# Optimization experiments

Hardware: AMD Instinct MI355X
Metric: run time of the kernel (lower is better)

The kernel has to match this reference:

```python
import jax, jax.numpy as jnp
import numpy as np

BN_EPS = 1e-5


def _gru(x, Wih, Whh, bih, bhh):
    # x: [B,S,D]; Wih: [3H,D]; Whh: [3H,H]; PyTorch gate order (r, z, n)
    B, S, D = x.shape
    H = Whh.shape[1]
    xg = jnp.einsum('bsd,gd->bsg', x, Wih) + bih  # [B,S,3H] precomputed input gates

    def step(h, xg_t):
        hg = h @ Whh.T + bhh
        xr, xz, xn = jnp.split(xg_t, 3, axis=-1)
        hr, hz, hn = jnp.split(hg, 3, axis=-1)
        r = jax.nn.sigmoid(xr + hr)
        z = jax.nn.sigmoid(xz + hz)
        n = jnp.tanh(xn + r * hn)
        h_new = (1.0 - z) * n + z * h
        return h_new, h_new

    h0 = jnp.zeros((B, H), x.dtype)
    _, hs = jax.lax.scan(step, h0, jnp.swapaxes(xg, 0, 1))  # [S,B,H]
    return jnp.swapaxes(hs, 0, 1)


def _lstm(x, Wih, Whh, bih, bhh):
    # x: [B,S,D]; PyTorch gate order (i, f, g, o)
    B, S, D = x.shape
    H = Whh.shape[1]
    xg = jnp.einsum('bsd,gd->bsg', x, Wih) + bih  # [B,S,4H]

    def step(carry, xg_t):
        h, c = carry
        g = xg_t + h @ Whh.T + bhh
        i, f, gg, o = jnp.split(g, 4, axis=-1)
        i = jax.nn.sigmoid(i)
        f = jax.nn.sigmoid(f)
        gg = jnp.tanh(gg)
        o = jax.nn.sigmoid(o)
        c_new = f * c + i * gg
        h_new = o * jnp.tanh(c_new)
        return (h_new, c_new), h_new

    h0 = jnp.zeros((B, H), x.dtype)
    c0 = jnp.zeros((B, H), x.dtype)
    _, hs = jax.lax.scan(step, (h0, c0), jnp.swapaxes(xg, 0, 1))
    return jnp.swapaxes(hs, 0, 1)


def setup_inputs() -> dict:
    key = jax.random.key(0)
    B, S, D, H = 64, 512, 40, 512
    ks = jax.random.split(key, 16)
    s_in = 1.0 / np.sqrt(H)

    def u(k, shape):
        return jax.random.uniform(k, shape, jnp.float32, -s_in, s_in)

    inp = {
        'x': jax.random.normal(ks[0], (B, S, D), jnp.float32),
        # rec1: GRU
        'gru_Wih': u(ks[1], (3 * H, D)),
        'gru_Whh': u(ks[2], (3 * H, H)),
        'gru_bih': u(ks[3], (3 * H,)),
        'gru_bhh': u(ks[4], (3 * H,)),
        # rec2: LSTM over [x, ssr] -> input D+1
        'lstm_Wih': u(ks[5], (4 * H, D + 1)),
        'lstm_Whh': u(ks[6], (4 * H, H)),
        'lstm_bih': u(ks[7], (4 * H,)),
        'lstm_bhh': u(ks[8], (4 * H,)),
        # fc1/fc2/fc3: hidden -> 1
        'fc1_w': u(ks[9], (1, H)), 'fc1_b': u(ks[10], (1,)),
        'fc2_w': u(ks[11], (1, H)), 'fc2_b': u(ks[12], (1,)),
        'fc3_w': u(ks[13], (1, H)), 'fc3_b': u(ks[14], (1,)),
        # BatchNorm1d affine params
        'bn_gamma': jnp.ones((H,), jnp.float32),
        'bn_beta': jnp.zeros((H,), jnp.float32),
    }
    return inp


def reference(x, gru_Wih, gru_Whh, gru_bih, gru_bhh,
              lstm_Wih, lstm_Whh, lstm_bih, lstm_bhh,
              fc1_w, fc1_b, fc2_w, fc2_b, fc3_w, fc3_b,
              bn_gamma, bn_beta):
    B, S, D = x.shape
    o1 = _gru(x, gru_Wih, gru_Whh, gru_bih, gru_bhh)  # [B,S,H]
    # BatchNorm1d (training mode): per-channel stats over (batch, time)
    mean = jnp.mean(o1, axis=(0, 1))
    var = jnp.mean((o1 - mean) ** 2, axis=(0, 1))
    o1 = (o1 - mean) * jax.lax.rsqrt(var + BN_EPS) * bn_gamma + bn_beta
    # gated scalar channel (dropout p=0 is identity)
    sr = jax.nn.relu(o1 @ fc1_w.T + fc1_b)            # [B,S,1]
    w = jnp.abs(jax.nn.sigmoid(o1 @ fc2_w.T + fc2_b))  # [B,S,1]
    ssr = sr * (w + 1.0)                              # [B,S,1]
    x2 = jnp.concatenate([x, ssr], axis=2)            # [B,S,D+1]
    o2 = _lstm(x2, lstm_Wih, lstm_Whh, lstm_bih, lstm_bhh)
    out = jax.nn.relu(o2 @ fc3_w.T + fc3_b)           # [B,S,1]
    return out, ssr
```

## Files before the change

kernel.cpp:

```cpp
#include <hip/hip_runtime.h>
#include <stdint.h>

#define MB 16
#define GW 16
#define NU 32
#define HD 512
#define SEQ 512
#define DX 40

using short8 = __attribute__((ext_vector_type(8))) short;
using f32x4  = __attribute__((ext_vector_type(4))) float;

__device__ __forceinline__ unsigned short f2bf(float f) {
  uint32_t u = __builtin_bit_cast(uint32_t, f);
  u += 0x7fffu + ((u >> 16) & 1u);
  return (unsigned short)(u >> 16);
}
__device__ __forceinline__ float sigm(float x) { return 1.0f / (1.0f + __expf(-x)); }


__global__ __launch_bounds__(512, 2) void gru_kernel(
    const float* __restrict__ x, const float* __restrict__ Wih,
    const float* __restrict__ Whh, const float* __restrict__ bih,
    const float* __restrict__ bhh, unsigned* __restrict__ flags,
    unsigned short* __restrict__ hbuf, float* __restrict__ o1,
    float* __restrict__ stats)
{
  const int wg = blockIdx.x & (GW - 1);
  const int g  = blockIdx.x >> 4;
  const int tid = threadIdx.x;
  const int wave = tid >> 6;
  const int lane = tid & 63;
  const int u0 = wg * NU;
  const int bg = g * MB;

  __shared__ unsigned short h_s[MB][520];
  __shared__ unsigned short x_s[MB][72];
  __shared__ float gate_s[3][MB][NU];
  __shared__ float xn_s[MB][NU];

  for (int i = tid; i < MB * 32; i += 512) x_s[i >> 5][40 + (i & 31)] = 0;

  short8 bfrag[18];
  const int myGate = wave >> 1;
  const int ut = wave & 1;
  const int kq = (lane >> 4) * 8;
  if (wave < 6) {
    const int row = myGate * HD + u0 + ut * 16 + (lane & 15);
    for (int kt = 0; kt < 16; ++kt) {
      const float* p = Whh + (size_t)row * HD + kt * 32 + kq;
      short8 f;
#pragma unroll
      for (int j = 0; j < 8; ++j) f[j] = (short)f2bf(p[j]);
      bfrag[kt] = f;
    }
    for (int kt = 16; kt < 18; ++kt) {
      short8 f;
#pragma unroll
      for (int j = 0; j < 8; ++j) {
        int c = kt * 32 + kq + j - HD;
        float v = (myGate < 2 && c < DX) ? Wih[(size_t)row * DX + c] : 0.0f;
        f[j] = (short)f2bf(v);
      }
      bfrag[kt] = f;
    }
  } else {
    const int row = 2 * HD + u0 + (wave - 6) * 16 + (lane & 15);
    for (int kt = 0; kt < 2; ++kt) {
      short8 f;
#pragma unroll
      for (int j = 0; j < 8; ++j) {
        int c = kt * 32 + kq + j;
        f[j] = (short)((c < DX) ? f2bf(Wih[(size_t)row * DX + c]) : 0);
      }
      bfrag[kt] = f;
    }
  }

  const int sb = tid >> 5;
  const int su = tid & 31;
  float hprev = 0.0f, ssum = 0.0f, ssq = 0.0f;
  const float b_r  = bih[u0 + su] + bhh[u0 + su];
  const float b_z  = bih[HD + u0 + su] + bhh[HD + u0 + su];
  const float b_in = bih[2 * HD + u0 + su];
  const float b_hn = bhh[2 * HD + u0 + su];

  unsigned* gf = flags + g * GW * 16;
  unsigned* myProdFlag = gf + ((tid & 127) >> 3) * 16;

  for (int t = 0; t < SEQ; ++t) {
    const unsigned long long* hin64 =
        (const unsigned long long*)(hbuf + ((size_t)g * 2 + (t & 1)) * MB * HD);
    uint32_t* hout32 =
        (uint32_t*)(hbuf + ((size_t)g * 2 + ((t + 1) & 1)) * MB * HD);

    {
      while (__hip_atomic_load(myProdFlag, __ATOMIC_RELAXED,
                               __HIP_MEMORY_SCOPE_AGENT) < (unsigned)t)
        __builtin_amdgcn_s_sleep(1);
#pragma unroll
      for (int it = 0; it < 4; ++it) {
        int q = it * 512 + tid;
        unsigned long long v = __hip_atomic_load(hin64 + q, __ATOMIC_RELAXED,
                                                 __HIP_MEMORY_SCOPE_AGENT);
        *(unsigned long long*)(&h_s[q >> 7][(q & 127) * 4]) = v;
      }
    }
    {
      int b = tid >> 5, c = tid & 31;
      const float* xr = x + ((size_t)(bg + b) * SEQ + t) * DX;
      x_s[b][c] = f2bf(xr[c]);
      if (c < 8) x_s[b][32 + c] = f2bf(xr[32 + c]);
    }
    __syncthreads();

    if (wave < 6) {
      const int m = lane & 15;
      f32x4 acc = {0.f, 0.f, 0.f, 0.f};
#pragma unroll
      for (int kt = 0; kt < 16; ++kt) {
        short8 a = *(const short8*)(&h_s[m][kt * 32 + kq]);
        acc = __builtin_amdgcn_mfma_f32_16x16x32_bf16(a, bfrag[kt], acc, 0, 0, 0);
      }
      short8 ax0 = *(const short8*)(&x_s[m][kq]);
      short8 ax1 = *(const short8*)(&x_s[m][32 + kq]);
      acc = __builtin_amdgcn_mfma_f32_16x16x32_bf16(ax0, bfrag[16], acc, 0, 0, 0);
      acc = __builtin_amdgcn_mfma_f32_16x16x32_bf16(ax1, bfrag[17], acc, 0, 0, 0);
#pragma unroll
      for (int r = 0; r < 4; ++r)
        gate_s[myGate][(lane >> 4) * 4 + r][ut * 16 + (lane & 15)] = acc[r];
    } else {
      const int m = lane & 15;
      f32x4 acc = {0.f, 0.f, 0.f, 0.f};
      short8 ax0 = *(const short8*)(&x_s[m][kq]);
      short8 ax1 = *(const short8*)(&x_s[m][32 + kq]);
      acc = __builtin_amdgcn_mfma_f32_16x16x32_bf16(ax0, bfrag[0], acc, 0, 0, 0);
      acc = __builtin_amdgcn_mfma_f32_16x16x32_bf16(ax1, bfrag[1], acc, 0, 0, 0);
#pragma unroll
      for (int r = 0; r < 4; ++r)
        xn_s[(lane >> 4) * 4 + r][(wave - 6) * 16 + (lane & 15)] = acc[r];
    }
    __syncthreads();

    float r_ = sigm(gate_s[0][sb][su] + b_r);
    float z_ = sigm(gate_s[1][sb][su] + b_z);
    float n_ = tanhf(xn_s[sb][su] + b_in + r_ * (gate_s[2][sb][su] + b_hn));
    float h = (1.0f - z_) * n_ + z_ * hprev;
    hprev = h;
    ssum += h; ssq += h * h;
    {
      float hp = __shfl_xor(h, 1);
      if ((tid & 1) == 0) {
        uint32_t packed = (uint32_t)f2bf(h) | ((uint32_t)f2bf(hp) << 16);
        __hip_atomic_store(hout32 + ((sb * HD + u0 + su) >> 1), packed,
                           __ATOMIC_RELAXED, __HIP_MEMORY_SCOPE_AGENT);
      }
    }
    __syncthreads();

    if (tid == 0)
      __hip_atomic_store(gf + wg * 16, (unsigned)(t + 1), __ATOMIC_RELAXED,
                         __HIP_MEMORY_SCOPE_AGENT);
    o1[((size_t)(bg + sb) * SEQ + t) * HD + u0 + su] = h;
  }

  atomicAdd(&stats[u0 + su], ssum);
  atomicAdd(&stats[HD + u0 + su], ssq);
}

__global__ __launch_bounds__(512, 2) void lstm_kernel(
    const float* __restrict__ x, const float* __restrict__ Wih,
    const float* __restrict__ Whh, const float* __restrict__ bih,
    const float* __restrict__ bhh, const float* __restrict__ ssr,
    unsigned* __restrict__ flags, unsigned short* __restrict__ hbuf,
    float* __restrict__ o2)
{
  const int wg = blockIdx.x & (GW - 1);
  const int g  = blockIdx.x >> 4;
  const int tid = threadIdx.x;
  const int wave = tid >> 6;
  const int lane = tid & 63;
  const int u0 = wg * NU;
  const int bg = g * MB;

  __shared__ unsigned short h_s[MB][520];
  __shared__ unsigned short x_s[MB][72];
  __shared__ float gate_s[4][MB][NU];

  for (int i = tid; i < MB * 32; i += 512) x_s[i >> 5][40 + (i & 31)] = 0;

  short8 bfrag[18];
  const int myGate = wave >> 1;
  const int ut = wave & 1;
  const int kq = (lane >> 4) * 8;
  {
    const int row = myGate * HD + u0 + ut * 16 + (lane & 15);
    for (int kt = 0; kt < 16; ++kt) {
      const float* p = Whh + (size_t)row * HD + kt * 32 + kq;
      short8 f;
#pragma unroll
      for (int j = 0; j < 8; ++j) f[j] = (short)f2bf(p[j]);
      bfrag[kt] = f;
    }
    for (int kt = 16; kt < 18; ++kt) {
      short8 f;
#pragma unroll
      for (int j = 0; j < 8; ++j) {
        int c = kt * 32 + kq + j - HD;
        float v = (c < 41) ? Wih[(size_t)row * 41 + c] : 0.0f;
        f[j] = (short)f2bf(v);
      }
      bfrag[kt] = f;
    }
  }

  const int sb = tid >> 5;
  const int su = tid & 31;
  float creg = 0.0f;
  const float b_i = bih[u0 + su] + bhh[u0 + su];
  const float b_f = bih[HD + u0 + su] + bhh[HD + u0 + su];
  const float b_g = bih[2 * HD + u0 + su] + bhh[2 * HD + u0 + su];
  const float b_o = bih[3 * HD + u0 + su] + bhh[3 * HD + u0 + su];

  unsigned* gf = flags + g * GW * 16;
  unsigned* myProdFlag = gf + ((tid & 127) >> 3) * 16;

  for (int t = 0; t < SEQ; ++t) {
    const unsigned long long* hin64 =
        (const unsigned long long*)(hbuf + ((size_t)g * 2 + (t & 1)) * MB * HD);
    uint32_t* hout32 =
        (uint32_t*)(hbuf + ((size_t)g * 2 + ((t + 1) & 1)) * MB * HD);

    {
      while (__hip_atomic_load(myProdFlag, __ATOMIC_RELAXED,
                               __HIP_MEMORY_SCOPE_AGENT) < (unsigned)t)
        __builtin_amdgcn_s_sleep(1);
#pragma unroll
      for (int it = 0; it < 4; ++it) {
        int q = it * 512 + tid;
        unsigned long long v = __hip_atomic_load(hin64 + q, __ATOMIC_RELAXED,
                                                 __HIP_MEMORY_SCOPE_AGENT);
        *(unsigned long long*)(&h_s[q >> 7][(q & 127) * 4]) = v;
      }
    }
    {
      int b = tid >> 5, c = tid & 31;
      const float* xr = x + ((size_t)(bg + b) * SEQ + t) * DX;
      x_s[b][c] = f2bf(xr[c]);
      if (c < 8) x_s[b][32 + c] = f2bf(xr[32 + c]);
      if (c == 8) x_s[b][40] = f2bf(ssr[(size_t)(bg + b) * SEQ + t]);
    }
    __syncthreads();

    {
      const int m = lane & 15;
      f32x4 acc = {0.f, 0.f, 0.f, 0.f};
#pragma unroll
      for (int kt = 0; kt < 16; ++kt) {
        short8 a = *(const short8*)(&h_s[m][kt * 32 + kq]);
        acc = __builtin_amdgcn_mfma_f32_16x16x32_bf16(a, bfrag[kt], acc, 0, 0, 0);
      }
      short8 ax0 = *(const short8*)(&x_s[m][kq]);
      short8 ax1 = *(const short8*)(&x_s[m][32 + kq]);
      acc = __builtin_amdgcn_mfma_f32_16x16x32_bf16(ax0, bfrag[16], acc, 0, 0, 0);
      acc = __builtin_amdgcn_mfma_f32_16x16x32_bf16(ax1, bfrag[17], acc, 0, 0, 0);
#pragma unroll
      for (int r = 0; r < 4; ++r)
        gate_s[myGate][(lane >> 4) * 4 + r][ut * 16 + (lane & 15)] = acc[r];
    }
    __syncthreads();

    float gi = sigm(gate_s[0][sb][su] + b_i);
    float gf_ = sigm(gate_s[1][sb][su] + b_f);
    float gg = tanhf(gate_s[2][sb][su] + b_g);
    float go = sigm(gate_s[3][sb][su] + b_o);
    creg = gf_ * creg + gi * gg;
    float h = go * tanhf(creg);
    {
      float hp = __shfl_xor(h, 1);
      if ((tid & 1) == 0) {
        uint32_t packed = (uint32_t)f2bf(h) | ((uint32_t)f2bf(hp) << 16);
        __hip_atomic_store(hout32 + ((sb * HD + u0 + su) >> 1), packed,
                           __ATOMIC_RELAXED, __HIP_MEMORY_SCOPE_AGENT);
      }
    }
    __syncthreads();

    if (tid == 0)
      __hip_atomic_store(gf + wg * 16, (unsigned)(t + 1), __ATOMIC_RELAXED,
                         __HIP_MEMORY_SCOPE_AGENT);
    o2[((size_t)(bg + sb) * SEQ + t) * HD + u0 + su] = h;
  }
}

__global__ __launch_bounds__(512) void coef_kernel(
    const float* __restrict__ stats, const float* __restrict__ fc1_w,
    const float* __restrict__ fc1_b, const float* __restrict__ fc2_w,
    const float* __restrict__ fc2_b, const float* __restrict__ gamma,
    const float* __restrict__ beta, float* __restrict__ coef)
{
  __shared__ float r1[512], r2[512];
  const int j = threadIdx.x;
  const float inv_n = 1.0f / 32768.0f;
  float mean = stats[j] * inv_n;
  float var = stats[HD + j] * inv_n - mean * mean;
  float scale = gamma[j] * rsqrtf(var + 1e-5f);
  float shift = beta[j] - mean * scale;
  coef[j] = fc1_w[j] * scale;
  coef[HD + j] = fc2_w[j] * scale;
  r1[j] = fc1_w[j] * shift;
  r2[j] = fc2_w[j] * shift;
  __syncthreads();
  for (int s = 256; s > 0; s >>= 1) {
    if (j < s) { r1[j] += r1[j + s]; r2[j] += r2[j + s]; }
    __syncthreads();
  }
  if (j == 0) {
    coef[2 * HD] = r1[0] + fc1_b[0];
    coef[2 * HD + 1] = r2[0] + fc2_b[0];
  }
}

__global__ __launch_bounds__(256) void ssr_kernel(
    const float* __restrict__ o1, const float* __restrict__ coef,
    float* __restrict__ ssr_ws, float* __restrict__ dssr)
{
  const int row = blockIdx.x * 4 + (threadIdx.x >> 6);
  const int lane = threadIdx.x & 63;
  const float* p = o1 + (size_t)row * HD + lane * 8;
  float s1 = 0.f, s2 = 0.f;
#pragma unroll
  for (int j = 0; j < 8; ++j) {
    float v = p[j];
    s1 += v * coef[lane * 8 + j];
    s2 += v * coef[HD + lane * 8 + j];
  }
#pragma unroll
  for (int off = 32; off > 0; off >>= 1) {
    s1 += __shfl_down(s1, off);
    s2 += __shfl_down(s2, off);
  }
  if (lane == 0) {
    float sr = fmaxf(s1 + coef[2 * HD], 0.0f);
    float w = fabsf(sigm(s2 + coef[2 * HD + 1]));
    float v = sr * (1.0f + w);
    ssr_ws[row] = v;
    dssr[row] = v;
  }
}

__global__ __launch_bounds__(256) void out_kernel(
    const float* __restrict__ o2, const float* __restrict__ fc3_w,
    const float* __restrict__ fc3_b, float* __restrict__ dout)
{
  const int row = blockIdx.x * 4 + (threadIdx.x >> 6);
  const int lane = threadIdx.x & 63;
  const float* p = o2 + (size_t)row * HD + lane * 8;
  float s = 0.f;
#pragma unroll
  for (int j = 0; j < 8; ++j) s += p[j] * fc3_w[lane * 8 + j];
#pragma unroll
  for (int off = 32; off > 0; off >>= 1) s += __shfl_down(s, off);
  if (lane == 0) dout[row] = fmaxf(s + fc3_b[0], 0.0f);
}

extern "C" void kernel_launch(void* const* d_in, const int* in_sizes, int n_in,
                              void* d_out, int out_size, void* d_ws, size_t ws_size,
                              hipStream_t stream) {
  (void)in_sizes; (void)n_in; (void)out_size; (void)ws_size;
  const float* x    = (const float*)d_in[0];
  const float* gWih = (const float*)d_in[1];
  const float* gWhh = (const float*)d_in[2];
  const float* gbih = (const float*)d_in[3];
  const float* gbhh = (const float*)d_in[4];
  const float* lWih = (const float*)d_in[5];
  const float* lWhh = (const float*)d_in[6];
  const float* lbih = (const float*)d_in[7];
  const float* lbhh = (const float*)d_in[8];
  const float* fc1w = (const float*)d_in[9];
  const float* fc1b = (const float*)d_in[10];
  const float* fc2w = (const float*)d_in[11];
  const float* fc2b = (const float*)d_in[12];
  const float* fc3w = (const float*)d_in[13];
  const float* fc3b = (const float*)d_in[14];
  const float* gam  = (const float*)d_in[15];
  const float* bet  = (const float*)d_in[16];
  float* out = (float*)d_out;

  char* ws = (char*)d_ws;
  unsigned* flags_g = (unsigned*)(ws + 0);
  unsigned* flags_l = (unsigned*)(ws + 4096);
  float* stats      = (float*)(ws + 8192);
  float* coef       = (float*)(ws + 16384);
  float* ssr_ws     = (float*)(ws + 32768);
  unsigned short* hbuf_g = (unsigned short*)(ws + 262144);
  unsigned short* hbuf_l = (unsigned short*)(ws + 393216);
  float* o1 = (float*)(ws + 1048576);
  float* o2 = o1 + (size_t)64 * SEQ * HD;

  hipMemsetAsync(ws, 0, 12288, stream);
  hipMemsetAsync(ws + 262144, 0, 262144, stream);

  gru_kernel<<<dim3(64), dim3(512), 0, stream>>>(x, gWih, gWhh, gbih, gbhh,
                                                 flags_g, hbuf_g, o1, stats);
  coef_kernel<<<dim3(1), dim3(512), 0, stream>>>(stats, fc1w, fc1b, fc2w, fc2b,
                                                 gam, bet, coef);
  ssr_kernel<<<dim3(8192), dim3(256), 0, stream>>>(o1, coef, ssr_ws, out + 32768);
  lstm_kernel<<<dim3(64), dim3(512), 0, stream>>>(x, lWih, lWhh, lbih, lbhh, ssr_ws,
                                                  flags_l, hbuf_l, o2);
  out_kernel<<<dim3(8192), dim3(256), 0, stream>>>(o2, fc3w, fc3b, out);
}
```

Before: 3.304 ms.

## Fuse gate computation per wave and use per-wave flags with double-buffered LDS

Restructures the GRU and LSTM recurrent kernels so each wave computes all gates for its 16 hidden units in registers. This removes the gate_s shared-memory round trip and one of the per-step block barriers. Each wave publishes its own completion flag after a vmcnt wait, instead of one flag per block after a barrier. h and x shared buffers are double-buffered so only one __syncthreads remains per step. The grid shrinks to 32 blocks of 256 threads, with more weight registers per thread, which lowers parallelism and adds more flags to poll.

```diff
diff --git a/kernel.cpp b/kernel.cpp
--- a/kernel.cpp
+++ b/kernel.cpp
@@ -2,14 +2,16 @@
 #include <stdint.h>
 
 #define MB 16
-#define GW 16
-#define NU 32
+#define GW 8
+#define NU 64
 #define HD 512
 #define SEQ 512
 #define DX 40
+#define NPROD 32
 
 using short8 = __attribute__((ext_vector_type(8))) short;
 using f32x4  = __attribute__((ext_vector_type(4))) float;
+typedef unsigned long long ull;
 
 __device__ __forceinline__ unsigned short f2bf(float f) {
   uint32_t u = __builtin_bit_cast(uint32_t, f);
@@ -17,9 +19,14 @@
   return (unsigned short)(u >> 16);
 }
 __device__ __forceinline__ float sigm(float x) { return 1.0f / (1.0f + __expf(-x)); }
-
-
-__global__ __launch_bounds__(512, 2) void gru_kernel(
+__device__ __forceinline__ ull pack4bf(float4 v) {
+  return (ull)f2bf(v.x) | ((ull)f2bf(v.y) << 16) | ((ull)f2bf(v.z) << 32) |
+         ((ull)f2bf(v.w) << 48);
+}
+#define MFMA(a, b, c) __builtin_amdgcn_mfma_f32_16x16x32_bf16((a), (b), (c), 0, 0, 0)
+
+
+__global__ __launch_bounds__(256, 1) void gru_kernel(
     const float* __restrict__ x, const float* __restrict__ Wih,
     const float* __restrict__ Whh, const float* __restrict__ bih,
     const float* __restrict__ bhh, unsigned* __restrict__ flags,
@@ -27,148 +34,138 @@
     float* __restrict__ stats)
 {
   const int wg = blockIdx.x & (GW - 1);
-  const int g  = blockIdx.x >> 4;
+  const int g  = blockIdx.x >> 3;
   const int tid = threadIdx.x;
   const int wave = tid >> 6;
   const int lane = tid & 63;
-  const int u0 = wg * NU;
+  const int n = lane & 15;
+  const int q = lane >> 4;
+  const int kq = q * 8;
+  const int u = wg * NU + wave * 16 + n;
   const int bg = g * MB;
 
-  __shared__ unsigned short h_s[MB][520];
-  __shared__ unsigned short x_s[MB][72];
-  __shared__ float gate_s[3][MB][NU];
-  __shared__ float xn_s[MB][NU];
-
-  for (int i = tid; i < MB * 32; i += 512) x_s[i >> 5][40 + (i & 31)] = 0;
-
-  short8 bfrag[18];
-  const int myGate = wave >> 1;
-  const int ut = wave & 1;
-  const int kq = (lane >> 4) * 8;
-  if (wave < 6) {
-    const int row = myGate * HD + u0 + ut * 16 + (lane & 15);
+  __shared__ unsigned short h_s[2][MB][520];
+  __shared__ unsigned short x_s[2][MB][72];
+
+  for (int i = tid; i < 2 * MB * 24; i += 256) {
+    int pbuf = i / (MB * 24), r = (i / 24) % MB, c = 40 + (i % 24);
+    x_s[pbuf][r][c] = 0;
+  }
+
+  short8 WR[16], WZ[16], WN[16], XR[2], XZ[2], XN[2];
+  for (int kt = 0; kt < 16; ++kt) {
+    const float* pr = Whh + (size_t)(0 * HD + u) * HD + kt * 32 + kq;
+    const float* pz = Whh + (size_t)(1 * HD + u) * HD + kt * 32 + kq;
+    const float* pn = Whh + (size_t)(2 * HD + u) * HD + kt * 32 + kq;
+    short8 fr, fz, fn;
+#pragma unroll
+    for (int j = 0; j < 8; ++j) {
+      fr[j] = (short)f2bf(pr[j]); fz[j] = (short)f2bf(pz[j]);
+      fn[j] = (short)f2bf(pn[j]);
+    }
+    WR[kt] = fr; WZ[kt] = fz; WN[kt] = fn;
+  }
+  for (int kt = 0; kt < 2; ++kt) {
+    short8 fr, fz, fn;
+#pragma unroll
+    for (int j = 0; j < 8; ++j) {
+      int c = kt * 32 + kq + j;
+      float vr = (c < DX) ? Wih[(size_t)(0 * HD + u) * DX + c] : 0.0f;
+      float vz = (c < DX) ? Wih[(size_t)(1 * HD + u) * DX + c] : 0.0f;
+      float vn = (c < DX) ? Wih[(size_t)(2 * HD + u) * DX + c] : 0.0f;
+      fr[j] = (short)f2bf(vr); fz[j] = (short)f2bf(vz); fn[j] = (short)f2bf(vn);
+    }
+    XR[kt] = fr; XZ[kt] = fz; XN[kt] = fn;
+  }
+
+  const float b_r  = bih[u] + bhh[u];
+  const float b_z  = bih[HD + u] + bhh[HD + u];
+  const float b_in = bih[2 * HD + u];
+  const float b_hn = bhh[2 * HD + u];
+
+  float hprev[4] = {0.f, 0.f, 0.f, 0.f};
+  float ssum = 0.f, ssq = 0.f;
+
+  unsigned* gflags   = flags + g * NPROD * 16;
+  unsigned* myflag   = gflags + (wg * 4 + wave) * 16;
+  unsigned* pollflag = gflags + (tid >> 3) * 16;
+  const int sp = tid >> 3;
+  const int sj = tid & 7;
+
+  for (int t = 0; t < SEQ; ++t) {
+    const int pb = t & 1;
+    const ull* hin = (const ull*)(hbuf + ((size_t)g * 2 + pb) * MB * HD);
+    unsigned short* hout = hbuf + ((size_t)g * 2 + (pb ^ 1)) * MB * HD;
+
+    while (__hip_atomic_load(pollflag, __ATOMIC_RELAXED,
+                             __HIP_MEMORY_SCOPE_AGENT) < (unsigned)t)
+      __builtin_amdgcn_s_sleep(1);
+    ull w[8];
+#pragma unroll
+    for (int r2 = 0; r2 < 2; ++r2)
+#pragma unroll
+      for (int c4 = 0; c4 < 4; ++c4)
+        w[r2 * 4 + c4] = __hip_atomic_load(
+            hin + (2 * sj + r2) * 128 + sp * 4 + c4, __ATOMIC_RELAXED,
+            __HIP_MEMORY_SCOPE_AGENT);
+#pragma unroll
+    for (int r2 = 0; r2 < 2; ++r2)
+#pragma unroll
+      for (int c4 = 0; c4 < 4; ++c4)
+        *(ull*)(&h_s[pb][2 * sj + r2][sp * 16 + c4 * 4]) = w[r2 * 4 + c4];
+    {
+      int b = tid >> 4, c = tid & 15;
+      if (c < 10) {
+        float4 v = *(const float4*)(x + ((size_t)(bg + b) * SEQ + t) * DX + c * 4);
+        *(ull*)(&x_s[pb][b][c * 4]) = pack4bf(v);
+      }
+    }
+    __syncthreads();
+
+    f32x4 aR = {0,0,0,0}, aZ = {0,0,0,0}, aN = {0,0,0,0}, aX = {0,0,0,0};
+#pragma unroll
     for (int kt = 0; kt < 16; ++kt) {
-      const float* p = Whh + (size_t)row * HD + kt * 32 + kq;
-      short8 f;
-#pragma unroll
-      for (int j = 0; j < 8; ++j) f[j] = (short)f2bf(p[j]);
-      bfrag[kt] = f;
-    }
-    for (int kt = 16; kt < 18; ++kt) {
-      short8 f;
-#pragma unroll
-      for (int j = 0; j < 8; ++j) {
-        int c = kt * 32 + kq + j - HD;
-        float v = (myGate < 2 && c < DX) ? Wih[(size_t)row * DX + c] : 0.0f;
-        f[j] = (short)f2bf(v);
-      }
-      bfrag[kt] = f;
-    }
-  } else {
-    const int row = 2 * HD + u0 + (wave - 6) * 16 + (lane & 15);
-    for (int kt = 0; kt < 2; ++kt) {
-      short8 f;
-#pragma unroll
-      for (int j = 0; j < 8; ++j) {
-        int c = kt * 32 + kq + j;
-        f[j] = (short)((c < DX) ? f2bf(Wih[(size_t)row * DX + c]) : 0);
-      }
-      bfrag[kt] = f;
-    }
-  }
-
-  const int sb = tid >> 5;
-  const int su = tid & 31;
-  float hprev = 0.0f, ssum = 0.0f, ssq = 0.0f;
-  const float b_r  = bih[u0 + su] + bhh[u0 + su];
-  const float b_z  = bih[HD + u0 + su] + bhh[HD + u0 + su];
-  const float b_in = bih[2 * HD + u0 + su];
-  const float b_hn = bhh[2 * HD + u0 + su];
-
-  unsigned* gf = flags + g * GW * 16;
-  unsigned* myProdFlag = gf + ((tid & 127) >> 3) * 16;
-
-  for (int t = 0; t < SEQ; ++t) {
-    const unsigned long long* hin64 =
-        (const unsigned long long*)(hbuf + ((size_t)g * 2 + (t & 1)) * MB * HD);
-    uint32_t* hout32 =
-        (uint32_t*)(hbuf + ((size_t)g * 2 + ((t + 1) & 1)) * MB * HD);
-
+      short8 a = *(const short8*)(&h_s[pb][n][kt * 32 + kq]);
+      aR = MFMA(a, WR[kt], aR);
+      aZ = MFMA(a, WZ[kt], aZ);
+      aN = MFMA(a, WN[kt], aN);
+    }
     {
-      while (__hip_atomic_load(myProdFlag, __ATOMIC_RELAXED,
-                               __HIP_MEMORY_SCOPE_AGENT) < (unsigned)t)
-        __builtin_amdgcn_s_sleep(1);
-#pragma unroll
-      for (int it = 0; it < 4; ++it) {
-        int q = it * 512 + tid;
-        unsigned long long v = __hip_atomic_load(hin64 + q, __ATOMIC_RELAXED,
-                                                 __HIP_MEMORY_SCOPE_AGENT);
-        *(unsigned long long*)(&h_s[q >> 7][(q & 127) * 4]) = v;
-      }
-    }
-    {
-      int b = tid >> 5, c = tid & 31;
-      const float* xr = x + ((size_t)(bg + b) * SEQ + t) * DX;
-      x_s[b][c] = f2bf(xr[c]);
-      if (c < 8) x_s[b][32 + c] = f2bf(xr[32 + c]);
-    }
-    __syncthreads();
-
-    if (wave < 6) {
-      const int m = lane & 15;
-      f32x4 acc = {0.f, 0.f, 0.f, 0.f};
-#pragma unroll
-      for (int kt = 0; kt < 16; ++kt) {
-        short8 a = *(const short8*)(&h_s[m][kt * 32 + kq]);
-        acc = __builtin_amdgcn_mfma_f32_16x16x32_bf16(a, bfrag[kt], acc, 0, 0, 0);
-      }
-      short8 ax0 = *(const short8*)(&x_s[m][kq]);
-      short8 ax1 = *(const short8*)(&x_s[m][32 + kq]);
-      acc = __builtin_amdgcn_mfma_f32_16x16x32_bf16(ax0, bfrag[16], acc, 0, 0, 0);
-      acc = __builtin_amdgcn_mfma_f32_16x16x32_bf16(ax1, bfrag[17], acc, 0, 0, 0);
-#pragma unroll
-      for (int r = 0; r < 4; ++r)
-        gate_s[myGate][(lane >> 4) * 4 + r][ut * 16 + (lane & 15)] = acc[r];
-    } else {
-      const int m = lane & 15;
-      f32x4 acc = {0.f, 0.f, 0.f, 0.f};
-      short8 ax0 = *(const short8*)(&x_s[m][kq]);
-      short8 ax1 = *(const short8*)(&x_s[m][32 + kq]);
-      acc = __builtin_amdgcn_mfma_f32_16x16x32_bf16(ax0, bfrag[0], acc, 0, 0, 0);
-      acc = __builtin_amdgcn_mfma_f32_16x16x32_bf16(ax1, bfrag[1], acc, 0, 0, 0);
-#pragma unroll
-      for (int r = 0; r < 4; ++r)
-        xn_s[(lane >> 4) * 4 + r][(wave - 6) * 16 + (lane & 15)] = acc[r];
-    }
-    __syncthreads();
-
-    float r_ = sigm(gate_s[0][sb][su] + b_r);
-    float z_ = sigm(gate_s[1][sb][su] + b_z);
-    float n_ = tanhf(xn_s[sb][su] + b_in + r_ * (gate_s[2][sb][su] + b_hn));
-    float h = (1.0f - z_) * n_ + z_ * hprev;
-    hprev = h;
-    ssum += h; ssq += h * h;
-    {
-      float hp = __shfl_xor(h, 1);
-      if ((tid & 1) == 0) {
-        uint32_t packed = (uint32_t)f2bf(h) | ((uint32_t)f2bf(hp) << 16);
-        __hip_atomic_store(hout32 + ((sb * HD + u0 + su) >> 1), packed,
-                           __ATOMIC_RELAXED, __HIP_MEMORY_SCOPE_AGENT);
-      }
-    }
-    __syncthreads();
-
-    if (tid == 0)
-      __hip_atomic_store(gf + wg * 16, (unsigned)(t + 1), __ATOMIC_RELAXED,
+      short8 a0 = *(const short8*)(&x_s[pb][n][kq]);
+      short8 a1 = *(const short8*)(&x_s[pb][n][32 + kq]);
+      aR = MFMA(a0, XR[0], aR); aR = MFMA(a1, XR[1], aR);
+      aZ = MFMA(a0, XZ[0], aZ); aZ = MFMA(a1, XZ[1], aZ);
+      aX = MFMA(a0, XN[0], aX); aX = MFMA(a1, XN[1], aX);
+    }
+
+    float hv[4];
+#pragma unroll
+    for (int r = 0; r < 4; ++r) {
+      float rr = sigm(aR[r] + b_r);
+      float zz = sigm(aZ[r] + b_z);
+      float nn = tanhf(aX[r] + b_in + rr * (aN[r] + b_hn));
+      float h = (1.0f - zz) * nn + zz * hprev[r];
+      hprev[r] = h; hv[r] = h;
+      ssum += h; ssq += h * h;
+    }
+#pragma unroll
+    for (int r = 0; r < 4; ++r)
+      __hip_atomic_store(hout + (q * 4 + r) * HD + u, f2bf(hv[r]),
+                         __ATOMIC_RELAXED, __HIP_MEMORY_SCOPE_AGENT);
+    asm volatile("s_waitcnt vmcnt(0)" ::: "memory");
+    if (lane == 0)
+      __hip_atomic_store(myflag, (unsigned)(t + 1), __ATOMIC_RELAXED,
                          __HIP_MEMORY_SCOPE_AGENT);
-    o1[((size_t)(bg + sb) * SEQ + t) * HD + u0 + su] = h;
-  }
-
-  atomicAdd(&stats[u0 + su], ssum);
-  atomicAdd(&stats[HD + u0 + su], ssq);
-}
-
-__global__ __launch_bounds__(512, 2) void lstm_kernel(
+#pragma unroll
+    for (int r = 0; r < 4; ++r)
+      o1[((size_t)(bg + q * 4 + r) * SEQ + t) * HD + u] = hv[r];
+  }
+
+  atomicAdd(&stats[u], ssum);
+  atomicAdd(&stats[HD + u], ssq);
+}
+
+__global__ __launch_bounds__(256, 1) void lstm_kernel(
     const float* __restrict__ x, const float* __restrict__ Wih,
     const float* __restrict__ Whh, const float* __restrict__ bih,
     const float* __restrict__ bhh, const float* __restrict__ ssr,
@@ -176,120 +173,138 @@
     float* __restrict__ o2)
 {
   const int wg = blockIdx.x & (GW - 1);
-  const int g  = blockIdx.x >> 4;
+  const int g  = blockIdx.x >> 3;
   const int tid = threadIdx.x;
   const int wave = tid >> 6;
   const int lane = tid & 63;
-  const int u0 = wg * NU;
+  const int n = lane & 15;
+  const int q = lane >> 4;
+  const int kq = q * 8;
+  const int u = wg * NU + wave * 16 + n;
   const int bg = g * MB;
 
-  __shared__ unsigned short h_s[MB][520];
-  __shared__ unsigned short x_s[MB][72];
-  __shared__ float gate_s[4][MB][NU];
-
-  for (int i = tid; i < MB * 32; i += 512) x_s[i >> 5][40 + (i & 31)] = 0;
-
-  short8 bfrag[18];
-  const int myGate = wave >> 1;
-  const int ut = wave & 1;
-  const int kq = (lane >> 4) * 8;
-  {
-    const int row = myGate * HD + u0 + ut * 16 + (lane & 15);
+  __shared__ unsigned short h_s[2][MB][520];
+  __shared__ unsigned short x_s[2][MB][72];
+
+  for (int i = tid; i < 2 * MB * 23; i += 256) {
+    int pbuf = i / (MB * 23), r = (i / 23) % MB, c = 41 + (i % 23);
+    x_s[pbuf][r][c] = 0;
+  }
+
+  short8 WI[16], WF[16], WG_[16], WO[16], XI[2], XF[2], XG[2], XO[2];
+  for (int kt = 0; kt < 16; ++kt) {
+    const float* pi = Whh + (size_t)(0 * HD + u) * HD + kt * 32 + kq;
+    const float* pf = Whh + (size_t)(1 * HD + u) * HD + kt * 32 + kq;
+    const float* pg = Whh + (size_t)(2 * HD + u) * HD + kt * 32 + kq;
+    const float* po = Whh + (size_t)(3 * HD + u) * HD + kt * 32 + kq;
+    short8 fi, ff, fg, fo;
+#pragma unroll
+    for (int j = 0; j < 8; ++j) {
+      fi[j] = (short)f2bf(pi[j]); ff[j] = (short)f2bf(pf[j]);
+      fg[j] = (short)f2bf(pg[j]); fo[j] = (short)f2bf(po[j]);
+    }
+    WI[kt] = fi; WF[kt] = ff; WG_[kt] = fg; WO[kt] = fo;
+  }
+  for (int kt = 0; kt < 2; ++kt) {
+    short8 fi, ff, fg, fo;
+#pragma unroll
+    for (int j = 0; j < 8; ++j) {
+      int c = kt * 32 + kq + j;
+      float vi = (c < 41) ? Wih[(size_t)(0 * HD + u) * 41 + c] : 0.0f;
+      float vf = (c < 41) ? Wih[(size_t)(1 * HD + u) * 41 + c] : 0.0f;
+      float vg = (c < 41) ? Wih[(size_t)(2 * HD + u) * 41 + c] : 0.0f;
+      float vo = (c < 41) ? Wih[(size_t)(3 * HD + u) * 41 + c] : 0.0f;
+      fi[j] = (short)f2bf(vi); ff[j] = (short)f2bf(vf);
+      fg[j] = (short)f2bf(vg); fo[j] = (short)f2bf(vo);
+    }
+    XI[kt] = fi; XF[kt] = ff; XG[kt] = fg; XO[kt] = fo;
+  }
+
+  const float b_i = bih[u] + bhh[u];
+  const float b_f = bih[HD + u] + bhh[HD + u];
+  const float b_g = bih[2 * HD + u] + bhh[2 * HD + u];
+  const float b_o = bih[3 * HD + u] + bhh[3 * HD + u];
+
+  float creg[4] = {0.f, 0.f, 0.f, 0.f};
+
+  unsigned* gflags   = flags + g * NPROD * 16;
+  unsigned* myflag   = gflags + (wg * 4 + wave) * 16;
+  unsigned* pollflag = gflags + (tid >> 3) * 16;
+  const int sp = tid >> 3;
+  const int sj = tid & 7;
+
+  for (int t = 0; t < SEQ; ++t) {
+    const int pb = t & 1;
+    const ull* hin = (const ull*)(hbuf + ((size_t)g * 2 + pb) * MB * HD);
+    unsigned short* hout = hbuf + ((size_t)g * 2 + (pb ^ 1)) * MB * HD;
+
+    while (__hip_atomic_load(pollflag, __ATOMIC_RELAXED,
+                             __HIP_MEMORY_SCOPE_AGENT) < (unsigned)t)
+      __builtin_amdgcn_s_sleep(1);
+    ull w[8];
+#pragma unroll
+    for (int r2 = 0; r2 < 2; ++r2)
+#pragma unroll
+      for (int c4 = 0; c4 < 4; ++c4)
+        w[r2 * 4 + c4] = __hip_atomic_load(
+            hin + (2 * sj + r2) * 128 + sp * 4 + c4, __ATOMIC_RELAXED,
+            __HIP_MEMORY_SCOPE_AGENT);
+#pragma unroll
+    for (int r2 = 0; r2 < 2; ++r2)
+#pragma unroll
+      for (int c4 = 0; c4 < 4; ++c4)
+        *(ull*)(&h_s[pb][2 * sj + r2][sp * 16 + c4 * 4]) = w[r2 * 4 + c4];
+    {
+      int b = tid >> 4, c = tid & 15;
+      if (c < 10) {
+        float4 v = *(const float4*)(x + ((size_t)(bg + b) * SEQ + t) * DX + c * 4);
+        *(ull*)(&x_s[pb][b][c * 4]) = pack4bf(v);
+      } else if (c == 10) {
+        x_s[pb][b][40] = f2bf(ssr[(size_t)(bg + b) * SEQ + t]);
+      }
+    }
+    __syncthreads();
+
+    f32x4 aI = {0,0,0,0}, aF = {0,0,0,0}, aG = {0,0,0,0}, aO = {0,0,0,0};
+#pragma unroll
     for (int kt = 0; kt < 16; ++kt) {
-      const float* p = Whh + (size_t)row * HD + kt * 32 + kq;
-      short8 f;
-#pragma unroll
-      for (int j = 0; j < 8; ++j) f[j] = (short)f2bf(p[j]);
-      bfrag[kt] = f;
-    }
-    for (int kt = 16; kt < 18; ++kt) {
-      short8 f;
-#pragma unroll
-      for (int j = 0; j < 8; ++j) {
-        int c = kt * 32 + kq + j - HD;
-        float v = (c < 41) ? Wih[(size_t)row * 41 + c] : 0.0f;
-        f[j] = (short)f2bf(v);
-      }
-      bfrag[kt] = f;
-    }
-  }
-
-  const int sb = tid >> 5;
-  const int su = tid & 31;
-  float creg = 0.0f;
-  const float b_i = bih[u0 + su] + bhh[u0 + su];
-  const float b_f = bih[HD + u0 + su] + bhh[HD + u0 + su];
-  const float b_g = bih[2 * HD + u0 + su] + bhh[2 * HD + u0 + su];
-  const float b_o = bih[3 * HD + u0 + su] + bhh[3 * HD + u0 + su];
-
-  unsigned* gf = flags + g * GW * 16;
-  unsigned* myProdFlag = gf + ((tid & 127) >> 3) * 16;
-
-  for (int t = 0; t < SEQ; ++t) {
-    const unsigned long long* hin64 =
-        (const unsigned long long*)(hbuf + ((size_t)g * 2 + (t & 1)) * MB * HD);
-    uint32_t* hout32 =
-        (uint32_t*)(hbuf + ((size_t)g * 2 + ((t + 1) & 1)) * MB * HD);
-
+      short8 a = *(const short8*)(&h_s[pb][n][kt * 32 + kq]);
+      aI = MFMA(a, WI[kt], aI);
+      aF = MFMA(a, WF[kt], aF);
+      aG = MFMA(a, WG_[kt], aG);
+      aO = MFMA(a, WO[kt], aO);
+    }
     {
-      while (__hip_atomic_load(myProdFlag, __ATOMIC_RELAXED,
-                               __HIP_MEMORY_SCOPE_AGENT) < (unsigned)t)
-        __builtin_amdgcn_s_sleep(1);
-#pragma unroll
-      for (int it = 0; it < 4; ++it) {
-        int q = it * 512 + tid;
-        unsigned long long v = __hip_atomic_load(hin64 + q, __ATOMIC_RELAXED,
-                                                 __HIP_MEMORY_SCOPE_AGENT);
-        *(unsigned long long*)(&h_s[q >> 7][(q & 127) * 4]) = v;
-      }
-    }
-    {
-      int b = tid >> 5, c = tid & 31;
-      const float* xr = x + ((size_t)(bg + b) * SEQ + t) * DX;
-      x_s[b][c] = f2bf(xr[c]);
-      if (c < 8) x_s[b][32 + c] = f2bf(xr[32 + c]);
-      if (c == 8) x_s[b][40] = f2bf(ssr[(size_t)(bg + b) * SEQ + t]);
-    }
-    __syncthreads();
-
-    {
-      const int m = lane & 15;
-      f32x4 acc = {0.f, 0.f, 0.f, 0.f};
-#pragma unroll
-      for (int kt = 0; kt < 16; ++kt) {
-        short8 a = *(const short8*)(&h_s[m][kt * 32 + kq]);
-        acc = __builtin_amdgcn_mfma_f32_16x16x32_bf16(a, bfrag[kt], acc, 0, 0, 0);
-      }
-      short8 ax0 = *(const short8*)(&x_s[m][kq]);
-      short8 ax1 = *(const short8*)(&x_s[m][32 + kq]);
-      acc = __builtin_amdgcn_mfma_f32_16x16x32_bf16(ax0, bfrag[16], acc, 0, 0, 0);
-      acc = __builtin_amdgcn_mfma_f32_16x16x32_bf16(ax1, bfrag[17], acc, 0, 0, 0);
-#pragma unroll
-      for (int r = 0; r < 4; ++r)
-        gate_s[myGate][(lane >> 4) * 4 + r][ut * 16 + (lane & 15)] = acc[r];
-    }
-    __syncthreads();
-
-    float gi = sigm(gate_s[0][sb][su] + b_i);
-    float gf_ = sigm(gate_s[1][sb][su] + b_f);
-    float gg = tanhf(gate_s[2][sb][su] + b_g);
-    float go = sigm(gate_s[3][sb][su] + b_o);
-    creg = gf_ * creg + gi * gg;
-    float h = go * tanhf(creg);
-    {
-      float hp = __shfl_xor(h, 1);
-      if ((tid & 1) == 0) {
-        uint32_t packed = (uint32_t)f2bf(h) | ((uint32_t)f2bf(hp) << 16);
-        __hip_atomic_store(hout32 + ((sb * HD + u0 + su) >> 1), packed,
-                           __ATOMIC_RELAXED, __HIP_MEMORY_SCOPE_AGENT);
-      }
-    }
-    __syncthreads();
-
-    if (tid == 0)
-      __hip_atomic_store(gf + wg * 16, (unsigned)(t + 1), __ATOMIC_RELAXED,
+      short8 a0 = *(const short8*)(&x_s[pb][n][kq]);
+      short8 a1 = *(const short8*)(&x_s[pb][n][32 + kq]);
+      aI = MFMA(a0, XI[0], aI); aI = MFMA(a1, XI[1], aI);
+      aF = MFMA(a0, XF[0], aF); aF = MFMA(a1, XF[1], aF);
+      aG = MFMA(a0, XG[0], aG); aG = MFMA(a1, XG[1], aG);
+      aO = MFMA(a0, XO[0], aO); aO = MFMA(a1, XO[1], aO);
+    }
+
+    float hv[4];
+#pragma unroll
+    for (int r = 0; r < 4; ++r) {
+      float gi = sigm(aI[r] + b_i);
+      float gf = sigm(aF[r] + b_f);
+      float gg = tanhf(aG[r] + b_g);
+      float go = sigm(aO[r] + b_o);
+      float c = gf * creg[r] + gi * gg;
+      creg[r] = c;
+      hv[r] = go * tanhf(c);
+    }
+#pragma unroll
+    for (int r = 0; r < 4; ++r)
+      __hip_atomic_store(hout + (q * 4 + r) * HD + u, f2bf(hv[r]),
+                         __ATOMIC_RELAXED, __HIP_MEMORY_SCOPE_AGENT);
+    asm volatile("s_waitcnt vmcnt(0)" ::: "memory");
+    if (lane == 0)
+      __hip_atomic_store(myflag, (unsigned)(t + 1), __ATOMIC_RELAXED,
                          __HIP_MEMORY_SCOPE_AGENT);
-    o2[((size_t)(bg + sb) * SEQ + t) * HD + u0 + su] = h;
+#pragma unroll
+    for (int r = 0; r < 4; ++r)
+      o2[((size_t)(bg + q * 4 + r) * SEQ + t) * HD + u] = hv[r];
   }
 }
 
@@ -389,24 +404,24 @@
 
   char* ws = (char*)d_ws;
   unsigned* flags_g = (unsigned*)(ws + 0);
-  unsigned* flags_l = (unsigned*)(ws + 4096);
-  float* stats      = (float*)(ws + 8192);
-  float* coef       = (float*)(ws + 16384);
+  unsigned* flags_l = (unsigned*)(ws + 8192);
+  float* stats      = (float*)(ws + 16384);
+  float* coef       = (float*)(ws + 24576);
   float* ssr_ws     = (float*)(ws + 32768);
   unsigned short* hbuf_g = (unsigned short*)(ws + 262144);
   unsigned short* hbuf_l = (unsigned short*)(ws + 393216);
   float* o1 = (float*)(ws + 1048576);
   float* o2 = o1 + (size_t)64 * SEQ * HD;
 
-  hipMemsetAsync(ws, 0, 12288, stream);
+  hipMemsetAsync(ws, 0, 20480, stream);
   hipMemsetAsync(ws + 262144, 0, 262144, stream);
 
-  gru_kernel<<<dim3(64), dim3(512), 0, stream>>>(x, gWih, gWhh, gbih, gbhh,
+  gru_kernel<<<dim3(32), dim3(256), 0, stream>>>(x, gWih, gWhh, gbih, gbhh,
                                                  flags_g, hbuf_g, o1, stats);
   coef_kernel<<<dim3(1), dim3(512), 0, stream>>>(stats, fc1w, fc1b, fc2w, fc2b,
                                                  gam, bet, coef);
   ssr_kernel<<<dim3(8192), dim3(256), 0, stream>>>(o1, coef, ssr_ws, out + 32768);
-  lstm_kernel<<<dim3(64), dim3(512), 0, stream>>>(x, lWih, lWhh, lbih, lbhh, ssr_ws,
+  lstm_kernel<<<dim3(32), dim3(256), 0, stream>>>(x, lWih, lWhh, lbih, lbhh, ssr_ws,
                                                   flags_l, hbuf_l, o2);
   out_kernel<<<dim3(8192), dim3(256), 0, stream>>>(o2, fc3w, fc3b, out);
 }
```

After: 7.693 ms. 2.33x slower.

## Use per-wave flags for fine-grained cross-block step synchronization in recurrent kernels

Applied to the files above, without the earlier changes.

Each wave now publishes its own progress flag right after its packed h stores drain, replacing the block-wide barrier and the single per-block flag set by thread 0. Each consumer thread polls only the flag of the producer wave whose h columns it reads, and loads a contiguous 16-element slice of the previous h. The x (and ssr) loads for the step are issued before the spin-wait so their latency overlaps the wait, and the first polls skip the sleep. The intent is to shorten the critical path of each recurrent step, at the cost of more flag memory, more flag polling traffic and reliance on vmcnt ordering for correctness.

```diff
diff --git a/kernel.cpp b/kernel.cpp
--- a/kernel.cpp
+++ b/kernel.cpp
@@ -10,6 +10,7 @@
 
 using short8 = __attribute__((ext_vector_type(8))) short;
 using f32x4  = __attribute__((ext_vector_type(4))) float;
+typedef unsigned long long ull;
 
 __device__ __forceinline__ unsigned short f2bf(float f) {
   uint32_t u = __builtin_bit_cast(uint32_t, f);
@@ -34,8 +35,8 @@
   const int u0 = wg * NU;
   const int bg = g * MB;
 
-  __shared__ unsigned short h_s[MB][520];
-  __shared__ unsigned short x_s[MB][72];
+  __shared__ __attribute__((aligned(16))) unsigned short h_s[MB][520];
+  __shared__ __attribute__((aligned(16))) unsigned short x_s[MB][72];
   __shared__ float gate_s[3][MB][NU];
   __shared__ float xn_s[MB][NU];
 
@@ -79,39 +80,46 @@
 
   const int sb = tid >> 5;
   const int su = tid & 31;
+  const int cb = tid & 31;
   float hprev = 0.0f, ssum = 0.0f, ssq = 0.0f;
   const float b_r  = bih[u0 + su] + bhh[u0 + su];
   const float b_z  = bih[HD + u0 + su] + bhh[HD + u0 + su];
   const float b_in = bih[2 * HD + u0 + su];
   const float b_hn = bhh[2 * HD + u0 + su];
 
-  unsigned* gf = flags + g * GW * 16;
-  unsigned* myProdFlag = gf + ((tid & 127) >> 3) * 16;
+  unsigned* gflags = flags + g * 128 * 16;
+  unsigned* myflag = gflags + (wg * 8 + wave) * 16;
+  unsigned* pollflag = gflags + (((cb >> 1) * 8) + (sb >> 1)) * 16;
 
   for (int t = 0; t < SEQ; ++t) {
-    const unsigned long long* hin64 =
-        (const unsigned long long*)(hbuf + ((size_t)g * 2 + (t & 1)) * MB * HD);
+    const ull* hin64 = (const ull*)(hbuf + ((size_t)g * 2 + (t & 1)) * MB * HD);
     uint32_t* hout32 =
         (uint32_t*)(hbuf + ((size_t)g * 2 + ((t + 1) & 1)) * MB * HD);
 
+    const float* xr = x + ((size_t)(bg + sb) * SEQ + t) * DX;
+    float xv0 = xr[su];
+    float xv1 = (su < 8) ? xr[32 + su] : 0.0f;
+
     {
-      while (__hip_atomic_load(myProdFlag, __ATOMIC_RELAXED,
+      int spin = 0;
+      while (__hip_atomic_load(pollflag, __ATOMIC_RELAXED,
                                __HIP_MEMORY_SCOPE_AGENT) < (unsigned)t)
-        __builtin_amdgcn_s_sleep(1);
-#pragma unroll
-      for (int it = 0; it < 4; ++it) {
-        int q = it * 512 + tid;
-        unsigned long long v = __hip_atomic_load(hin64 + q, __ATOMIC_RELAXED,
-                                                 __HIP_MEMORY_SCOPE_AGENT);
-        *(unsigned long long*)(&h_s[q >> 7][(q & 127) * 4]) = v;
-      }
-    }
-    {
-      int b = tid >> 5, c = tid & 31;
-      const float* xr = x + ((size_t)(bg + b) * SEQ + t) * DX;
-      x_s[b][c] = f2bf(xr[c]);
-      if (c < 8) x_s[b][32 + c] = f2bf(xr[32 + c]);
-    }
+        if (++spin > 2) __builtin_amdgcn_s_sleep(1);
+      ull w0 = __hip_atomic_load(hin64 + sb * 128 + cb * 4 + 0, __ATOMIC_RELAXED,
+                                 __HIP_MEMORY_SCOPE_AGENT);
+      ull w1 = __hip_atomic_load(hin64 + sb * 128 + cb * 4 + 1, __ATOMIC_RELAXED,
+                                 __HIP_MEMORY_SCOPE_AGENT);
+      ull w2 = __hip_atomic_load(hin64 + sb * 128 + cb * 4 + 2, __ATOMIC_RELAXED,
+                                 __HIP_MEMORY_SCOPE_AGENT);
+      ull w3 = __hip_atomic_load(hin64 + sb * 128 + cb * 4 + 3, __ATOMIC_RELAXED,
+                                 __HIP_MEMORY_SCOPE_AGENT);
+      *(ull*)(&h_s[sb][cb * 16 + 0])  = w0;
+      *(ull*)(&h_s[sb][cb * 16 + 4])  = w1;
+      *(ull*)(&h_s[sb][cb * 16 + 8])  = w2;
+      *(ull*)(&h_s[sb][cb * 16 + 12]) = w3;
+    }
+    x_s[sb][su] = f2bf(xv0);
+    if (su < 8) x_s[sb][32 + su] = f2bf(xv1);
     __syncthreads();
 
     if (wave < 6) {
@@ -119,8 +127,8 @@
       f32x4 acc = {0.f, 0.f, 0.f, 0.f};
 #pragma unroll
       for (int kt = 0; kt < 16; ++kt) {
-        short8 a = *(const short8*)(&h_s[m][kt * 32 + kq]);
-        acc = __builtin_amdgcn_mfma_f32_16x16x32_bf16(a, bfrag[kt], acc, 0, 0, 0);
+        short8 av = *(const short8*)(&h_s[m][kt * 32 + kq]);
+        acc = __builtin_amdgcn_mfma_f32_16x16x32_bf16(av, bfrag[kt], acc, 0, 0, 0);
       }
       short8 ax0 = *(const short8*)(&x_s[m][kq]);
       short8 ax1 = *(const short8*)(&x_s[m][32 + kq]);
@@ -155,12 +163,11 @@
         __hip_atomic_store(hout32 + ((sb * HD + u0 + su) >> 1), packed,
                            __ATOMIC_RELAXED, __HIP_MEMORY_SCOPE_AGENT);
       }
-    }
-    __syncthreads();
-
-    if (tid == 0)
-      __hip_atomic_store(gf + wg * 16, (unsigned)(t + 1), __ATOMIC_RELAXED,
-                         __HIP_MEMORY_SCOPE_AGENT);
+      asm volatile("s_waitcnt vmcnt(0)" ::: "memory");
+      if (lane == 0)
+        __hip_atomic_store(myflag, (unsigned)(t + 1), __ATOMIC_RELAXED,
+                           __HIP_MEMORY_SCOPE_AGENT);
+    }
     o1[((size_t)(bg + sb) * SEQ + t) * HD + u0 + su] = h;
   }
 
@@ -183,11 +190,11 @@
   const int u0 = wg * NU;
   const int bg = g * MB;
 
-  __shared__ unsigned short h_s[MB][520];
-  __shared__ unsigned short x_s[MB][72];
+  __shared__ __attribute__((aligned(16))) unsigned short h_s[MB][520];
+  __shared__ __attribute__((aligned(16))) unsigned short x_s[MB][72];
   __shared__ float gate_s[4][MB][NU];
 
-  for (int i = tid; i < MB * 32; i += 512) x_s[i >> 5][40 + (i & 31)] = 0;
+  for (int i = tid; i < MB * 23; i += 512) x_s[i / 23][41 + (i % 23)] = 0;
 
   short8 bfrag[18];
   const int myGate = wave >> 1;
@@ -216,40 +223,48 @@
 
   const int sb = tid >> 5;
   const int su = tid & 31;
+  const int cb = tid & 31;
   float creg = 0.0f;
   const float b_i = bih[u0 + su] + bhh[u0 + su];
   const float b_f = bih[HD + u0 + su] + bhh[HD + u0 + su];
   const float b_g = bih[2 * HD + u0 + su] + bhh[2 * HD + u0 + su];
   const float b_o = bih[3 * HD + u0 + su] + bhh[3 * HD + u0 + su];
 
-  unsigned* gf = flags + g * GW * 16;
-  unsigned* myProdFlag = gf + ((tid & 127) >> 3) * 16;
+  unsigned* gflags = flags + g * 128 * 16;
+  unsigned* myflag = gflags + (wg * 8 + wave) * 16;
+  unsigned* pollflag = gflags + (((cb >> 1) * 8) + (sb >> 1)) * 16;
 
   for (int t = 0; t < SEQ; ++t) {
-    const unsigned long long* hin64 =
-        (const unsigned long long*)(hbuf + ((size_t)g * 2 + (t & 1)) * MB * HD);
+    const ull* hin64 = (const ull*)(hbuf + ((size_t)g * 2 + (t & 1)) * MB * HD);
     uint32_t* hout32 =
         (uint32_t*)(hbuf + ((size_t)g * 2 + ((t + 1) & 1)) * MB * HD);
 
+    const float* xr = x + ((size_t)(bg + sb) * SEQ + t) * DX;
+    float xv0 = xr[su];
+    float xv1 = (su < 8) ? xr[32 + su] : 0.0f;
+    float sv = (su == 8) ? ssr[(size_t)(bg + sb) * SEQ + t] : 0.0f;
+
     {
-      while (__hip_atomic_load(myProdFlag, __ATOMIC_RELAXED,
+      int spin = 0;
+      while (__hip_atomic_load(pollflag, __ATOMIC_RELAXED,
                                __HIP_MEMORY_SCOPE_AGENT) < (unsigned)t)
-        __builtin_amdgcn_s_sleep(1);
-#pragma unroll
-      for (int it = 0; it < 4; ++it) {
-        int q = it * 512 + tid;
-        unsigned long long v = __hip_atomic_load(hin64 + q, __ATOMIC_RELAXED,
-                                                 __HIP_MEMORY_SCOPE_AGENT);
-        *(unsigned long long*)(&h_s[q >> 7][(q & 127) * 4]) = v;
-      }
-    }
-    {
-      int b = tid >> 5, c = tid & 31;
-      const float* xr = x + ((size_t)(bg + b) * SEQ + t) * DX;
-      x_s[b][c] = f2bf(xr[c]);
-      if (c < 8) x_s[b][32 + c] = f2bf(xr[32 + c]);
-      if (c == 8) x_s[b][40] = f2bf(ssr[(size_t)(bg + b) * SEQ + t]);
-    }
+        if (++spin > 2) __builtin_amdgcn_s_sleep(1);
+      ull w0 = __hip_atomic_load(hin64 + sb * 128 + cb * 4 + 0, __ATOMIC_RELAXED,
+                                 __HIP_MEMORY_SCOPE_AGENT);
+      ull w1 = __hip_atomic_load(hin64 + sb * 128 + cb * 4 + 1, __ATOMIC_RELAXED,
+                                 __HIP_MEMORY_SCOPE_AGENT);
+      ull w2 = __hip_atomic_load(hin64 + sb * 128 + cb * 4 + 2, __ATOMIC_RELAXED,
+                                 __HIP_MEMORY_SCOPE_AGENT);
+      ull w3 = __hip_atomic_load(hin64 + sb * 128 + cb * 4 + 3, __ATOMIC_RELAXED,
+                                 __HIP_MEMORY_SCOPE_AGENT);
+      *(ull*)(&h_s[sb][cb * 16 + 0])  = w0;
+      *(ull*)(&h_s[sb][cb * 16 + 4])  = w1;
+      *(ull*)(&h_s[sb][cb * 16 + 8])  = w2;
+      *(ull*)(&h_s[sb][cb * 16 + 12]) = w3;
+    }
+    x_s[sb][su] = f2bf(xv0);
+    if (su < 8) x_s[sb][32 + su] = f2bf(xv1);
+    if (su == 8) x_s[sb][40] = f2bf(sv);
     __syncthreads();
 
     {
@@ -257,8 +272,8 @@
       f32x4 acc = {0.f, 0.f, 0.f, 0.f};
 #pragma unroll
       for (int kt = 0; kt < 16; ++kt) {
-        short8 a = *(const short8*)(&h_s[m][kt * 32 + kq]);
-        acc = __builtin_amdgcn_mfma_f32_16x16x32_bf16(a, bfrag[kt], acc, 0, 0, 0);
+        short8 av = *(const short8*)(&h_s[m][kt * 32 + kq]);
+        acc = __builtin_amdgcn_mfma_f32_16x16x32_bf16(av, bfrag[kt], acc, 0, 0, 0);
       }
       short8 ax0 = *(const short8*)(&x_s[m][kq]);
       short8 ax1 = *(const short8*)(&x_s[m][32 + kq]);
@@ -283,12 +298,11 @@
         __hip_atomic_store(hout32 + ((sb * HD + u0 + su) >> 1), packed,
                            __ATOMIC_RELAXED, __HIP_MEMORY_SCOPE_AGENT);
       }
-    }
-    __syncthreads();
-
-    if (tid == 0)
-      __hip_atomic_store(gf + wg * 16, (unsigned)(t + 1), __ATOMIC_RELAXED,
-                         __HIP_MEMORY_SCOPE_AGENT);
+      asm volatile("s_waitcnt vmcnt(0)" ::: "memory");
+      if (lane == 0)
+        __hip_atomic_store(myflag, (unsigned)(t + 1), __ATOMIC_RELAXED,
+                           __HIP_MEMORY_SCOPE_AGENT);
+    }
     o2[((size_t)(bg + sb) * SEQ + t) * HD + u0 + su] = h;
   }
 }
@@ -389,16 +403,16 @@
 
   char* ws = (char*)d_ws;
   unsigned* flags_g = (unsigned*)(ws + 0);
-  unsigned* flags_l = (unsigned*)(ws + 4096);
-  float* stats      = (float*)(ws + 8192);
-  float* coef       = (float*)(ws + 16384);
-  float* ssr_ws     = (float*)(ws + 32768);
+  unsigned* flags_l = (unsigned*)(ws + 32768);
+  float* stats      = (float*)(ws + 65536);
+  float* coef       = (float*)(ws + 73728);
+  float* ssr_ws     = (float*)(ws + 81920);
   unsigned short* hbuf_g = (unsigned short*)(ws + 262144);
   unsigned short* hbuf_l = (unsigned short*)(ws + 393216);
   float* o1 = (float*)(ws + 1048576);
   float* o2 = o1 + (size_t)64 * SEQ * HD;
 
-  hipMemsetAsync(ws, 0, 12288, stream);
+  hipMemsetAsync(ws, 0, 69632, stream);
   hipMemsetAsync(ws + 262144, 0, 262144, stream);
 
   gru_kernel<<<dim3(64), dim3(512), 0, stream>>>(x, gWih, gWhh, gbih, gbhh,
```

Result: no change. 3.315 ms (+0.3%).
